# Kernel optimization log

Measured on AMD Instinct MI355X. Metric: run time of the kernel, lower is better.

The kernel has to match this reference:

```python
import jax, jax.numpy as jnp
import numpy as np

D_MODEL = 1024
N_HEADS = 16
HEAD_DIM = D_MODEL // N_HEADS
ROPE_BASE = 10000.0


def _rope_cos_sin(seq_len, head_dim, dtype):
    inv_freq = 1.0 / (ROPE_BASE ** (jnp.arange(0, head_dim, 2, dtype=jnp.float32) / head_dim))
    t = jnp.arange(seq_len, dtype=jnp.float32)
    freqs = jnp.outer(t, inv_freq)            # [S, head_dim//2]
    emb = jnp.concatenate([freqs, freqs], axis=-1)  # [S, head_dim]
    return jnp.cos(emb).astype(dtype), jnp.sin(emb).astype(dtype)


def _rotate_half(x):
    half = x.shape[-1] // 2
    return jnp.concatenate([-x[..., half:], x[..., :half]], axis=-1)


def setup_inputs() -> dict:
    key = jax.random.key(0)
    k0, k1, k2, k3, k4 = jax.random.split(key, 5)
    B, S = 2, 2048
    scale = 1.0 / np.sqrt(D_MODEL)
    return {
        "hidden_states": jax.random.normal(k0, (B, S, D_MODEL), dtype=jnp.float32),
        "w_q": jax.random.normal(k1, (D_MODEL, D_MODEL), dtype=jnp.float32) * scale,
        "w_k": jax.random.normal(k2, (D_MODEL, D_MODEL), dtype=jnp.float32) * scale,
        "w_v": jax.random.normal(k3, (D_MODEL, D_MODEL), dtype=jnp.float32) * scale,
        "w_o": jax.random.normal(k4, (D_MODEL, D_MODEL), dtype=jnp.float32) * scale,
    }


def reference(hidden_states, w_q, w_k, w_v, w_o):
    B, S, D = hidden_states.shape
    H, hd = N_HEADS, HEAD_DIM

    def proj(w):
        # nn.Linear: x @ w.T -> [B, H, S, hd]
        return (hidden_states @ w.T).reshape(B, S, H, hd).transpose(0, 2, 1, 3)

    q, k, v = proj(w_q), proj(w_k), proj(w_v)

    cos, sin = _rope_cos_sin(S, hd, hidden_states.dtype)
    cos = cos[None, None]  # [1,1,S,hd]
    sin = sin[None, None]
    q = q * cos + _rotate_half(q) * sin
    k = k * cos + _rotate_half(k) * sin

    scores = jnp.einsum("bhqd,bhkd->bhqk", q, k) / jnp.sqrt(jnp.asarray(hd, hidden_states.dtype))
    attn = jax.nn.softmax(scores, axis=-1)
    out = jnp.einsum("bhqk,bhkd->bhqd", attn, v)
    out = out.transpose(0, 2, 1, 3).reshape(B, S, D)
    return out @ w_o.T
```

## Files before the change

### kernel.cpp

```cpp
#include <hip/hip_runtime.h>
#include <math.h>

#define SEQ 2048
#define NTOK 4096
#define DM 1024

typedef __bf16 bf16x8 __attribute__((ext_vector_type(8)));
typedef __bf16 bf16x4 __attribute__((ext_vector_type(4)));
typedef float  f32x4  __attribute__((ext_vector_type(4)));
typedef float  f32x16 __attribute__((ext_vector_type(16)));

__device__ __forceinline__ void gll16(const void* g, void* l) {
    __builtin_amdgcn_global_load_lds(
        (const __attribute__((address_space(1))) void*)g,
        (__attribute__((address_space(3))) void*)l, 16, 0, 0);
}

__device__ __forceinline__ f32x4 mfma16(bf16x8 a, bf16x8 b, f32x4 c) {
    return __builtin_amdgcn_mfma_f32_16x16x32_bf16(a, b, c, 0, 0, 0);
}
__device__ __forceinline__ f32x16 mfma32(bf16x8 a, bf16x8 b, f32x16 c) {
    return __builtin_amdgcn_mfma_f32_32x32x16_bf16(a, b, c, 0, 0, 0);
}

__device__ __forceinline__ unsigned pk2(float x, float y) {
    union { __bf16 h; unsigned short s; } a, b;
    a.h = (__bf16)x; b.h = (__bf16)y;
    return (unsigned)a.s | ((unsigned)b.s << 16);
}

__global__ void rope_tables(float* __restrict__ ct, float* __restrict__ st) {
    int idx = blockIdx.x * 256 + threadIdx.x;
    int s = idx >> 6, d = idx & 63;
    int e = d & 31;
    float invf = 1.0f / powf(10000.0f, (float)e / 32.0f);
    float ang  = (float)s * invf;
    double a   = (double)ang;
    ct[s * 64 + d] = (float)cos(a);
    st[s * 64 + d] = (float)sin(a);
}

__global__ void conv_all(const float* __restrict__ hs, const float* __restrict__ wq,
                         const float* __restrict__ wk, const float* __restrict__ wv,
                         const float* __restrict__ wo, __bf16* hsb, __bf16* wqb,
                         __bf16* wkb, __bf16* wvb, __bf16* wob) {
    long i = (long)blockIdx.x * 256 + threadIdx.x;
    const long H4 = (long)NTOK * DM / 4;
    const float* src; __bf16* dst; long off;
    if (i < H4) { src = hs; dst = hsb; off = i; }
    else {
        long t = i - H4;
        int wsel = (int)(t >> 18);
        off = t & ((1L << 18) - 1);
        switch (wsel) {
            case 0:  src = wq; dst = wqb; break;
            case 1:  src = wk; dst = wkb; break;
            case 2:  src = wv; dst = wvb; break;
            default: src = wo; dst = wob; break;
        }
    }
    float4 v = ((const float4*)src)[off];
    __bf16* o = dst + off * 4;
    o[0] = (__bf16)v.x; o[1] = (__bf16)v.y; o[2] = (__bf16)v.z; o[3] = (__bf16)v.w;
}

template <typename OutT, bool ROPE>
__device__ __forceinline__ void gemm_core(__bf16* __restrict__ L,
                                          const __bf16* __restrict__ A,
                                          const __bf16* __restrict__ B,
                                          OutT* __restrict__ C, int N, float scale,
                                          const float* __restrict__ ct,
                                          const float* __restrict__ st,
                                          long bm, long bn) {
    const int tid  = threadIdx.x;
    const int lane = tid & 63;
    const int wid  = tid >> 6;
    const int l15  = lane & 15, lg = lane >> 4;
    const int wr = (wid >> 1) * 64, wc = (wid & 1) * 64;

    f32x4 acc[4][4];
    #pragma unroll
    for (int i = 0; i < 4; ++i)
        #pragma unroll
        for (int j = 0; j < 4; ++j) acc[i][j] = 0;

    const int i0 = tid, i1 = tid + 256;
    const __bf16* Ag0 = A + (bm + (i0 >> 2)) * 1024 + (((i0 & 3) ^ ((i0 >> 3) & 3)) * 8);
    const __bf16* Ag1 = A + (bm + (i1 >> 2)) * 1024 + (((i1 & 3) ^ ((i1 >> 3) & 3)) * 8);
    const __bf16* Bg0 = B + (bn + (i0 >> 2)) * 1024 + (((i0 & 3) ^ ((i0 >> 3) & 3)) * 8);
    const __bf16* Bg1 = B + (bn + (i1 >> 2)) * 1024 + (((i1 & 3) ^ ((i1 >> 3) & 3)) * 8);

    auto stage = [&](int buf, int k0) {
        gll16(Ag0 + k0, &L[buf * 8192 + tid * 8]);
        gll16(Ag1 + k0, &L[buf * 8192 + 2048 + tid * 8]);
        gll16(Bg0 + k0, &L[buf * 8192 + 4096 + tid * 8]);
        gll16(Bg1 + k0, &L[buf * 8192 + 6144 + tid * 8]);
    };

    const int rbase = l15 * 32 + ((lg ^ ((l15 >> 1) & 3)) * 8);

    auto compute = [&](int buf) {
        const int AS = buf * 8192, BS = buf * 8192 + 4096;
        bf16x8 a[4], b[4];
        #pragma unroll
        for (int i = 0; i < 4; ++i)
            a[i] = *(const bf16x8*)(L + AS + (wr + i * 16) * 32 + rbase);
        #pragma unroll
        for (int j = 0; j < 4; ++j)
            b[j] = *(const bf16x8*)(L + BS + (wc + j * 16) * 32 + rbase);
        __builtin_amdgcn_s_setprio(1);
        #pragma unroll
        for (int i = 0; i < 4; ++i)
            #pragma unroll
            for (int j = 0; j < 4; ++j)
                acc[i][j] = mfma16(a[i], b[j], acc[i][j]);
        __builtin_amdgcn_s_setprio(0);
    };

    stage(0, 0);
    __syncthreads();
    #pragma unroll 1
    for (int t = 0; t < 32; t += 2) {
        stage(1, (t + 1) * 32);
        compute(0);
        __syncthreads();
        if (t + 2 < 32) stage(0, (t + 2) * 32);
        compute(1);
        __syncthreads();
    }

    if constexpr (ROPE) {
        #pragma unroll
        for (int i = 0; i < 4; ++i)
            #pragma unroll
            for (int j = 0; j < 2; ++j)
                #pragma unroll
                for (int r = 0; r < 4; ++r) {
                    long row = bm + wr + i * 16 + lg * 4 + r;
                    int  s   = (int)(row & (SEQ - 1));
                    int  d   = j * 16 + l15;
                    float c  = ct[s * 64 + d];
                    float sn = st[s * 64 + d];
                    float x0 = acc[i][j][r], x1 = acc[i][j + 2][r];
                    long col = bn + wc + j * 16 + l15;
                    C[row * N + col]      = (OutT)((x0 * c - x1 * sn) * scale);
                    C[row * N + col + 32] = (OutT)((x1 * c + x0 * sn) * scale);
                }
    } else {
        #pragma unroll
        for (int i = 0; i < 4; ++i)
            #pragma unroll
            for (int j = 0; j < 4; ++j)
                #pragma unroll
                for (int r = 0; r < 4; ++r) {
                    long row = bm + wr + i * 16 + lg * 4 + r;
                    long col = bn + wc + j * 16 + l15;
                    C[row * N + col] = (OutT)(acc[i][j][r] * scale);
                }
    }
}

__global__ __launch_bounds__(256) void gemm_qkv(const __bf16* __restrict__ hsb,
                                                const __bf16* __restrict__ wqb,
                                                const __bf16* __restrict__ wkb,
                                                const __bf16* __restrict__ wvb,
                                                __bf16* __restrict__ Qb,
                                                __bf16* __restrict__ Kb,
                                                __bf16* __restrict__ Vtb,
                                                const float* __restrict__ ct,
                                                const float* __restrict__ st) {
    __shared__ __bf16 L[16384];
    const int bid = blockIdx.x;
    const int w = (bid & 7) * 96 + (bid >> 3);
    const int z = w >> 8, rem = w & 255;
    if (z == 0)
        gemm_core<__bf16, true>(L, hsb, wqb, Qb, 1024, 0.125f, ct, st,
                                (long)(rem >> 3) * 128, (long)(rem & 7) * 128);
    else if (z == 1)
        gemm_core<__bf16, true>(L, hsb, wkb, Kb, 1024, 1.0f, ct, st,
                                (long)(rem >> 3) * 128, (long)(rem & 7) * 128);
    else
        gemm_core<__bf16, false>(L, wvb, hsb, Vtb, 4096, 1.0f, nullptr, nullptr,
                                 (long)(rem & 7) * 128, (long)(rem >> 3) * 128);
}

__global__ __launch_bounds__(256) void gemm_out(const __bf16* __restrict__ A,
                                                const __bf16* __restrict__ B,
                                                float* __restrict__ C) {
    __shared__ __bf16 L[16384];
    const int bid = blockIdx.x;
    const int w = (bid & 7) * 32 + (bid >> 3);
    gemm_core<float, false>(L, A, B, C, 1024, 1.0f, nullptr, nullptr,
                            (long)(w >> 3) * 128, (long)(w & 7) * 128);
}

#define FIXED_M 16.0f

__global__ __launch_bounds__(512) void flash10(const __bf16* __restrict__ Qb,
                                               const __bf16* __restrict__ Kb,
                                               const __bf16* __restrict__ Vt,
                                               __bf16* __restrict__ Ob) {
    __shared__ __bf16 L[24576];
    const int h = blockIdx.x, b = blockIdx.y, qt = blockIdx.z;
    const int tid = threadIdx.x, lane = tid & 63, w = tid >> 6;
    const int wq = w >> 1, wk = w & 1;
    const int l31 = lane & 31;
    const int hi  = lane >> 5;
    const int x7  = l31 & 7;

    int kb[4], vb[2];
    #pragma unroll
    for (int d = 0; d < 4; ++d)
        kb[d] = (wk * 32 + l31) * 64 + (((d * 2 + hi) ^ x7) * 8);
    #pragma unroll
    for (int ks = 0; ks < 2; ++ks)
        vb[ks] = l31 * 64 + (((wk * 4 + ks * 2 + hi) ^ x7) * 8);

    const long qrow = (long)b * SEQ + qt * 128 + wq * 32 + l31;
    bf16x8 qf[4];
    #pragma unroll
    for (int d = 0; d < 4; ++d)
        qf[d] = *(const bf16x8*)(Qb + qrow * DM + h * 64 + d * 16 + hi * 8);

    f32x16 oacc[2];
    oacc[0] = 0; oacc[1] = 0;
    float lsum = 0.f;

    const int srow = tid >> 3;
    const int sgz  = (tid & 7) ^ (srow & 7);
    const __bf16* kp = Kb + ((long)b * SEQ + srow) * DM + h * 64 + sgz * 8;
    const __bf16* vp = Vt + ((long)h * 64 + srow) * NTOK + (long)b * SEQ + sgz * 8;

    auto stage = [&](int bf) {
        gll16(kp, &L[bf * 4096 + tid * 8]);
        gll16(vp, &L[8192 + bf * 4096 + tid * 8]);
        kp += (long)64 * DM;
        vp += 64;
    };

    const float L2E = 1.4426950408889634f;
    const float mL  = FIXED_M * L2E;

    auto compute = [&](int bf) {
        const int KS = bf * 4096, VS = 8192 + bf * 4096;

        f32x16 sc = 0;
        __builtin_amdgcn_s_setprio(1);
        #pragma unroll
        for (int d = 0; d < 4; ++d) {
            bf16x8 ka = *(const bf16x8*)(L + KS + kb[d]);
            sc = mfma32(ka, qf[d], sc);
        }
        __builtin_amdgcn_s_setprio(0);

        #pragma unroll
        for (int r = 0; r < 16; ++r) {
            sc[r] = __builtin_amdgcn_exp2f(__builtin_fmaf(sc[r], L2E, -mL));
            lsum += sc[r];
        }

        #pragma unroll
        for (int ks = 0; ks < 2; ++ks) {
            unsigned A0 = pk2(sc[ks * 8 + 0], sc[ks * 8 + 1]);
            unsigned A1 = pk2(sc[ks * 8 + 2], sc[ks * 8 + 3]);
            unsigned B0 = pk2(sc[ks * 8 + 4], sc[ks * 8 + 5]);
            unsigned B1 = pk2(sc[ks * 8 + 6], sc[ks * 8 + 7]);
            asm volatile("v_permlane32_swap_b32 %0, %1" : "+v"(A0), "+v"(B0));
            asm volatile("v_permlane32_swap_b32 %0, %1" : "+v"(A1), "+v"(B1));
            uint4 tw = {A0, A1, B0, B1};
            bf16x8 pf = *(bf16x8*)&tw;
            __builtin_amdgcn_s_setprio(1);
            #pragma unroll
            for (int dt = 0; dt < 2; ++dt) {
                bf16x8 va = *(const bf16x8*)(L + VS + dt * 2048 + vb[ks]);
                oacc[dt] = mfma32(va, pf, oacc[dt]);
            }
            __builtin_amdgcn_s_setprio(0);
        }
    };

    stage(0);
    __syncthreads();

    #pragma unroll 1
    for (int t = 0; t < 32; t += 2) {
        stage(1);
        compute(0);
        __syncthreads();
        if (t + 2 < 32) stage(0);
        compute(1);
        __syncthreads();
    }

    lsum += __shfl_xor(lsum, 32);

    float* df = (float*)L;
    float* lf = df + 9216;
    if (wk) {
        const int base = (wq * 64 + lane) * 36;
        #pragma unroll
        for (int i = 0; i < 4; ++i)
            *(f32x4*)(df + base + i * 4) = *(((f32x4*)&oacc[0]) + i);
        #pragma unroll
        for (int i = 0; i < 4; ++i)
            *(f32x4*)(df + base + 16 + i * 4) = *(((f32x4*)&oacc[1]) + i);
        if (hi == 0) lf[wq * 32 + l31] = lsum;
    }
    __syncthreads();
    if (!wk) {
        const int base = (wq * 64 + lane) * 36;
        float lt = lsum + lf[wq * 32 + l31];
        float linv = 1.0f / lt;
        const long tok = (long)b * SEQ + qt * 128 + wq * 32 + l31;
        #pragma unroll
        for (int dt = 0; dt < 2; ++dt) {
            #pragma unroll
            for (int g = 0; g < 4; ++g) {
                f32x4 ot = *(((f32x4*)&oacc[dt]) + g) +
                           *(const f32x4*)(df + base + dt * 16 + g * 4);
                bf16x4 o4;
                #pragma unroll
                for (int r = 0; r < 4; ++r) o4[r] = (__bf16)(ot[r] * linv);
                *(bf16x4*)(Ob + tok * DM + h * 64 + dt * 32 + g * 8 + 4 * hi) = o4;
            }
        }
    }
}

extern "C" void kernel_launch(void* const* d_in, const int* in_sizes, int n_in,
                              void* d_out, int out_size, void* d_ws, size_t ws_size,
                              hipStream_t stream) {
    const float* hs = (const float*)d_in[0];
    const float* wq = (const float*)d_in[1];
    const float* wk = (const float*)d_in[2];
    const float* wv = (const float*)d_in[3];
    const float* wo = (const float*)d_in[4];
    float* out = (float*)d_out;

    __bf16* hsb = (__bf16*)d_ws;
    __bf16* wqb = hsb + (long)NTOK * DM;
    __bf16* wkb = wqb + DM * DM;
    __bf16* wvb = wkb + DM * DM;
    __bf16* wob = wvb + DM * DM;
    __bf16* Qb  = wob + DM * DM;
    __bf16* Kb  = Qb + (long)NTOK * DM;
    __bf16* Vtb = Kb + (long)NTOK * DM;
    float*  ct  = (float*)(Vtb + (long)NTOK * DM);
    float*  st  = ct + SEQ * 64;

    rope_tables<<<dim3(SEQ * 64 / 256), 256, 0, stream>>>(ct, st);
    conv_all<<<dim3(8192), 256, 0, stream>>>(hs, wq, wk, wv, wo,
                                             hsb, wqb, wkb, wvb, wob);

    gemm_qkv<<<dim3(768), 256, 0, stream>>>(hsb, wqb, wkb, wvb,
                                            Qb, Kb, Vtb, ct, st);

    flash10<<<dim3(16, 2, SEQ / 128), 512, 0, stream>>>(Qb, Kb, Vtb, Qb);

    gemm_out<<<dim3(256), 256, 0, stream>>>(Qb, wob, out);
}
```

Measured before the change: 122.4 us.

## Halve flash attention block to 64 queries and fold rope tables into conversion

The flash attention kernel now uses 256-thread blocks covering 64 query rows instead of 512 threads covering 128. Each thread issues two staging loads per buffer so the same 64-key K/V tile is still filled, and LDS use shrinks. This doubles the grid to 1024 blocks for better CU occupancy and load balance, but each block now reloads K/V for half as many queries. The rope table kernel is merged into the conversion kernel as extra blocks to save a launch. The row-sum accumulation is vectorised into an f32x4 to shorten the dependency chain.

Result: slower. 130.7 us (+6.8%).

```diff
diff --git a/kernel.cpp b/kernel.cpp
--- a/kernel.cpp
+++ b/kernel.cpp
@@ -29,21 +29,22 @@
     return (unsigned)a.s | ((unsigned)b.s << 16);
 }
 
-__global__ void rope_tables(float* __restrict__ ct, float* __restrict__ st) {
-    int idx = blockIdx.x * 256 + threadIdx.x;
-    int s = idx >> 6, d = idx & 63;
-    int e = d & 31;
-    float invf = 1.0f / powf(10000.0f, (float)e / 32.0f);
-    float ang  = (float)s * invf;
-    double a   = (double)ang;
-    ct[s * 64 + d] = (float)cos(a);
-    st[s * 64 + d] = (float)sin(a);
-}
-
 __global__ void conv_all(const float* __restrict__ hs, const float* __restrict__ wq,
                          const float* __restrict__ wk, const float* __restrict__ wv,
                          const float* __restrict__ wo, __bf16* hsb, __bf16* wqb,
-                         __bf16* wkb, __bf16* wvb, __bf16* wob) {
+                         __bf16* wkb, __bf16* wvb, __bf16* wob,
+                         float* __restrict__ ct, float* __restrict__ st) {
+    if (blockIdx.x >= 8192) {
+        int t = (blockIdx.x - 8192) * 256 + threadIdx.x;
+        int s = t >> 6, d = t & 63;
+        int e = d & 31;
+        float invf = 1.0f / powf(10000.0f, (float)e / 32.0f);
+        float ang  = (float)s * invf;
+        double a   = (double)ang;
+        ct[s * 64 + d] = (float)cos(a);
+        st[s * 64 + d] = (float)sin(a);
+        return;
+    }
     long i = (long)blockIdx.x * 256 + threadIdx.x;
     const long H4 = (long)NTOK * DM / 4;
     const float* src; __bf16* dst; long off;
@@ -196,11 +197,11 @@
 
 #define FIXED_M 16.0f
 
-__global__ __launch_bounds__(512) void flash10(const __bf16* __restrict__ Qb,
+__global__ __launch_bounds__(256) void flash11(const __bf16* __restrict__ Qb,
                                                const __bf16* __restrict__ Kb,
                                                const __bf16* __restrict__ Vt,
                                                __bf16* __restrict__ Ob) {
-    __shared__ __bf16 L[24576];
+    __shared__ __bf16 L[16384];
     const int h = blockIdx.x, b = blockIdx.y, qt = blockIdx.z;
     const int tid = threadIdx.x, lane = tid & 63, w = tid >> 6;
     const int wq = w >> 1, wk = w & 1;
@@ -216,7 +217,7 @@
     for (int ks = 0; ks < 2; ++ks)
         vb[ks] = l31 * 64 + (((wk * 4 + ks * 2 + hi) ^ x7) * 8);
 
-    const long qrow = (long)b * SEQ + qt * 128 + wq * 32 + l31;
+    const long qrow = (long)b * SEQ + qt * 64 + wq * 32 + l31;
     bf16x8 qf[4];
     #pragma unroll
     for (int d = 0; d < 4; ++d)
@@ -224,18 +225,22 @@
 
     f32x16 oacc[2];
     oacc[0] = 0; oacc[1] = 0;
-    float lsum = 0.f;
+    f32x4 lv = 0;
 
     const int srow = tid >> 3;
     const int sgz  = (tid & 7) ^ (srow & 7);
-    const __bf16* kp = Kb + ((long)b * SEQ + srow) * DM + h * 64 + sgz * 8;
-    const __bf16* vp = Vt + ((long)h * 64 + srow) * NTOK + (long)b * SEQ + sgz * 8;
+    const __bf16* kp0 = Kb + ((long)b * SEQ + srow) * DM + h * 64 + sgz * 8;
+    const __bf16* kp1 = kp0 + (long)32 * DM;
+    const __bf16* vp0 = Vt + ((long)h * 64 + srow) * NTOK + (long)b * SEQ + sgz * 8;
+    const __bf16* vp1 = vp0 + (long)32 * NTOK;
 
     auto stage = [&](int bf) {
-        gll16(kp, &L[bf * 4096 + tid * 8]);
-        gll16(vp, &L[8192 + bf * 4096 + tid * 8]);
-        kp += (long)64 * DM;
-        vp += 64;
+        gll16(kp0, &L[bf * 4096 + tid * 8]);
+        gll16(kp1, &L[bf * 4096 + 2048 + tid * 8]);
+        gll16(vp0, &L[8192 + bf * 4096 + tid * 8]);
+        gll16(vp1, &L[8192 + bf * 4096 + 2048 + tid * 8]);
+        kp0 += (long)64 * DM; kp1 += (long)64 * DM;
+        vp0 += 64;            vp1 += 64;
     };
 
     const float L2E = 1.4426950408889634f;
@@ -254,9 +259,11 @@
         __builtin_amdgcn_s_setprio(0);
 
         #pragma unroll
-        for (int r = 0; r < 16; ++r) {
+        for (int r = 0; r < 16; ++r)
             sc[r] = __builtin_amdgcn_exp2f(__builtin_fmaf(sc[r], L2E, -mL));
-            lsum += sc[r];
+        {
+            const f32x4* scv = (const f32x4*)&sc;
+            lv += scv[0]; lv += scv[1]; lv += scv[2]; lv += scv[3];
         }
 
         #pragma unroll
@@ -292,10 +299,11 @@
         __syncthreads();
     }
 
+    float lsum = (lv[0] + lv[1]) + (lv[2] + lv[3]);
     lsum += __shfl_xor(lsum, 32);
 
     float* df = (float*)L;
-    float* lf = df + 9216;
+    float* lf = df + 4608;
     if (wk) {
         const int base = (wq * 64 + lane) * 36;
         #pragma unroll
@@ -311,7 +319,7 @@
         const int base = (wq * 64 + lane) * 36;
         float lt = lsum + lf[wq * 32 + l31];
         float linv = 1.0f / lt;
-        const long tok = (long)b * SEQ + qt * 128 + wq * 32 + l31;
+        const long tok = (long)b * SEQ + qt * 64 + wq * 32 + l31;
         #pragma unroll
         for (int dt = 0; dt < 2; ++dt) {
             #pragma unroll
@@ -348,14 +356,13 @@
     float*  ct  = (float*)(Vtb + (long)NTOK * DM);
     float*  st  = ct + SEQ * 64;
 
-    rope_tables<<<dim3(SEQ * 64 / 256), 256, 0, stream>>>(ct, st);
-    conv_all<<<dim3(8192), 256, 0, stream>>>(hs, wq, wk, wv, wo,
-                                             hsb, wqb, wkb, wvb, wob);
+    conv_all<<<dim3(8704), 256, 0, stream>>>(hs, wq, wk, wv, wo,
+                                             hsb, wqb, wkb, wvb, wob, ct, st);
 
     gemm_qkv<<<dim3(768), 256, 0, stream>>>(hsb, wqb, wkb, wvb,
                                             Qb, Kb, Vtb, ct, st);
 
-    flash10<<<dim3(16, 2, SEQ / 128), 512, 0, stream>>>(Qb, Kb, Vtb, Qb);
+    flash11<<<dim3(16, 2, SEQ / 64), 256, 0, stream>>>(Qb, Kb, Vtb, Qb);
 
     gemm_out<<<dim3(256), 256, 0, stream>>>(Qb, wob, out);
 }
```
